# Kernel tuning notes

Measured on AMD Instinct MI355X. Metric: run time of the kernel, lower is better.

## Reference

```python
import jax, jax.numpy as jnp
import numpy as np

B, S, H = 4, 2048, 768          # batch, seq, hidden
NH, HD = 12, 64                 # heads, head dim
R = 4                           # channel_shrink_ratio
LH, LHD = H // R, HD // R       # layout hidden (192), layout head dim (16)


def setup_inputs() -> dict:
    key = jax.random.key(0)
    ks = jax.random.split(key, 14)
    s = 0.02
    return {
        "hidden_states": jax.random.normal(ks[0], (B, S, H), jnp.float32),
        "layout_inputs": jax.random.normal(ks[1], (B, S, LH), jnp.float32),
        # text-stream projections (stored as [in, out], i.e. torch weight transposed)
        "Wq": jax.random.normal(ks[2], (H, H), jnp.float32) * s,
        "bq": jnp.zeros((H,), jnp.float32),
        "Wk": jax.random.normal(ks[3], (H, H), jnp.float32) * s,
        "bk": jnp.zeros((H,), jnp.float32),
        "Wv": jax.random.normal(ks[4], (H, H), jnp.float32) * s,
        "bv": jnp.zeros((H,), jnp.float32),
        # layout-stream projections
        "lWq": jax.random.normal(ks[5], (LH, LH), jnp.float32) * s,
        "lbq": jnp.zeros((LH,), jnp.float32),
        "lWk": jax.random.normal(ks[6], (LH, LH), jnp.float32) * s,
        "lbk": jnp.zeros((LH,), jnp.float32),
        "lWv": jax.random.normal(ks[7], (LH, LH), jnp.float32) * s,
        "lbv": jnp.zeros((LH,), jnp.float32),
    }


def _heads(x, w, b, hd):
    # [B,S,D_in] @ [D_in,D_out] -> [B, NH, S, hd]
    y = x @ w + b
    return y.reshape(x.shape[0], x.shape[1], NH, hd).transpose(0, 2, 1, 3)


def reference(hidden_states, layout_inputs, Wq, bq, Wk, bk, Wv, bv,
              lWq, lbq, lWk, lbk, lWv, lbv):
    q = _heads(hidden_states, Wq, bq, HD)
    k = _heads(hidden_states, Wk, bk, HD)
    v = _heads(hidden_states, Wv, bv, HD)
    lq = _heads(layout_inputs, lWq, lbq, LHD)
    lk = _heads(layout_inputs, lWk, lbk, LHD)
    lv = _heads(layout_inputs, lWv, lbv, LHD)

    # two QK^T score matrices, scaled then cross-added (both streams see the sum)
    scores = jnp.einsum('bhqd,bhkd->bhqk', q, k) / np.float32(HD) ** 0.5
    lscores = jnp.einsum('bhqd,bhkd->bhqk', lq, lk) / np.float32(LHD) ** 0.5
    combined = scores + lscores  # identical for both streams (no mask path)

    probs = jax.nn.softmax(combined, axis=-1)
    lprobs = jax.nn.softmax(combined, axis=-1)

    ctx = jnp.einsum('bhqk,bhkd->bhqd', probs, v)
    lctx = jnp.einsum('bhqk,bhkd->bhqd', lprobs, lv)

    ctx = ctx.transpose(0, 2, 1, 3).reshape(B, S, H)
    lctx = lctx.transpose(0, 2, 1, 3).reshape(B, S, LH)
    return ctx, lctx
```

## Files before the change

kernel.cpp:

```cpp
#include <hip/hip_runtime.h>
#include <cstdint>
#include <cstddef>

#define NB 4
#define NS 2048
#define NHH 12
#define DH 80
#define HT 768
#define HL 192

typedef __bf16 bf16x8 __attribute__((ext_vector_type(8)));
typedef float f32x4 __attribute__((ext_vector_type(4)));
typedef unsigned short u16x4 __attribute__((ext_vector_type(4)));

__device__ __forceinline__ unsigned short f2bf(float f) {
  union { float f; uint32_t u; } v; v.f = f;
  uint32_t u = v.u + 0x7FFF + ((v.u >> 16) & 1);
  return (unsigned short)(u >> 16);
}

__device__ __forceinline__ f32x4 mfma_bf16(bf16x8 a, bf16x8 b, f32x4 c) {
  return __builtin_amdgcn_mfma_f32_16x16x32_bf16(a, b, c, 0, 0, 0);
}

__device__ __forceinline__ void gl_lds(const unsigned short* g, unsigned short* l) {
  __builtin_amdgcn_global_load_lds(
      (const __attribute__((address_space(1))) uint32_t*)g,
      (__attribute__((address_space(3))) uint32_t*)l, 16, 0, 0);
}

__global__ __launch_bounds__(256) void k_prep(
    const float* __restrict__ hs, const float* __restrict__ li,
    const float* __restrict__ Wq, const float* __restrict__ Wk, const float* __restrict__ Wv,
    const float* __restrict__ lWq, const float* __restrict__ lWk, const float* __restrict__ lWv,
    unsigned short* __restrict__ Xb, unsigned short* __restrict__ Xlb,
    unsigned short* __restrict__ WtQ, unsigned short* __restrict__ WtK,
    unsigned short* __restrict__ WtV, unsigned short* __restrict__ WtLQ,
    unsigned short* __restrict__ WtLK, unsigned short* __restrict__ WtLV) {
  int blk = blockIdx.x, tid = threadIdx.x;
  if (blk < 7680) {
    const float* src; unsigned short* dst; int i;
    if (blk < 6144) { src = hs; dst = Xb;  i = blk * 256 + tid; }
    else            { src = li; dst = Xlb; i = (blk - 6144) * 256 + tid; }
    float4 v = *(const float4*)(src + (size_t)i * 4);
    u16x4 o; o[0] = f2bf(v.x); o[1] = f2bf(v.y); o[2] = f2bf(v.z); o[3] = f2bf(v.w);
    *(u16x4*)(dst + (size_t)i * 4) = o;
  } else {
    const float* w; unsigned short* wt; int i, K;
    if      (blk < 9984)  { w = Wq;  wt = WtQ;  i = (blk - 7680)  * 256 + tid; K = 768; }
    else if (blk < 12288) { w = Wk;  wt = WtK;  i = (blk - 9984)  * 256 + tid; K = 768; }
    else if (blk < 14592) { w = Wv;  wt = WtV;  i = (blk - 12288) * 256 + tid; K = 768; }
    else if (blk < 14736) { w = lWq; wt = WtLQ; i = (blk - 14592) * 256 + tid; K = 192; }
    else if (blk < 14880) { w = lWk; wt = WtLK; i = (blk - 14736) * 256 + tid; K = 192; }
    else                  { w = lWv; wt = WtLV; i = (blk - 14880) * 256 + tid; K = 192; }
    int n = i / K, k = i - n * K;
    wt[i] = f2bf(w[(size_t)k * K + n]);
  }
}

struct ProjArgs {
  const unsigned short* Wt[3];
  const float* bias[3];
  unsigned short* dst[3];
  float scale[3];
  int mode[3];
};

__global__ __launch_bounds__(256, 4) void k_proj3(
    const unsigned short* __restrict__ Xb, ProjArgs pa,
    int K, int hdshift, int dofs) {
  __shared__ unsigned short Xs[128 * 72];
  __shared__ unsigned short Ws[64 * 72];
  int z = blockIdx.z;
  const unsigned short* Wt = pa.Wt[z];
  int m0 = blockIdx.x * 128, n0 = blockIdx.y * 64;
  int tid = threadIdx.x;
  int lane = tid & 63, wave = tid >> 6, quad = lane >> 4, l16 = lane & 15;

  f32x4 acc[2][4];
#pragma unroll
  for (int mt = 0; mt < 2; ++mt)
#pragma unroll
    for (int nt = 0; nt < 4; ++nt) {
      acc[mt][nt][0] = 0.f; acc[mt][nt][1] = 0.f;
      acc[mt][nt][2] = 0.f; acc[mt][nt][3] = 0.f;
    }

  for (int kk = 0; kk < K; kk += 64) {
#pragma unroll
    for (int p = 0; p < 5; ++p) {
      int i = p * 256 + tid;
      if (i < 1152) {
        int r = i / 9, c = i - r * 9;
        const unsigned short* src = Xb + (size_t)(m0 + r) * K + kk + (c == 8 ? 0 : c * 8);
        gl_lds(src, Xs + i * 8);
      }
    }
#pragma unroll
    for (int p = 0; p < 3; ++p) {
      int i = p * 256 + tid;
      if (i < 576) {
        int r = i / 9, c = i - r * 9;
        const unsigned short* src = Wt + (size_t)(n0 + r) * K + kk + (c == 8 ? 0 : c * 8);
        gl_lds(src, Ws + i * 8);
      }
    }
    __syncthreads();

#pragma unroll
    for (int kc = 0; kc < 2; ++kc) {
      bf16x8 a0 = *(const bf16x8*)&Xs[(wave * 32 + l16) * 72 + kc * 32 + quad * 8];
      bf16x8 a1 = *(const bf16x8*)&Xs[(wave * 32 + 16 + l16) * 72 + kc * 32 + quad * 8];
#pragma unroll
      for (int nt = 0; nt < 4; ++nt) {
        bf16x8 b = *(const bf16x8*)&Ws[(nt * 16 + l16) * 72 + kc * 32 + quad * 8];
        acc[0][nt] = mfma_bf16(a0, b, acc[0][nt]);
        acc[1][nt] = mfma_bf16(a1, b, acc[1][nt]);
      }
    }
    __syncthreads();
  }

  const float* bias = pa.bias[z];
  unsigned short* dst = pa.dst[z];
  float scale = pa.scale[z];
  int mode = pa.mode[z];
  int hdm = (1 << hdshift) - 1;
#pragma unroll
  for (int mt = 0; mt < 2; ++mt) {
#pragma unroll
    for (int nt = 0; nt < 4; ++nt) {
      int n = n0 + nt * 16 + l16;
      float bv = bias[n];
      int mbase = m0 + wave * 32 + mt * 16 + quad * 4;
      int h = n >> hdshift, d = n & hdm;
      if (mode == 0) {
#pragma unroll
        for (int r = 0; r < 4; ++r) {
          int m = mbase + r;
          int b = m >> 11, s = m & (NS - 1);
          float y = (acc[mt][nt][r] + bv) * scale;
          dst[((size_t)(b * NHH + h) * NS + s) * DH + dofs + d] = f2bf(y);
        }
      } else {
        int b = mbase >> 11, s = mbase & (NS - 1);
        u16x4 pk;
#pragma unroll
        for (int r = 0; r < 4; ++r) pk[r] = f2bf((acc[mt][nt][r] + bv) * scale);
        *(u16x4*)(dst + ((size_t)(b * NHH + h) * DH + dofs + d) * NS + s) = pk;
      }
    }
  }
}

__global__ __launch_bounds__(256, 3) void k_attn(
    const unsigned short* __restrict__ Qg, const unsigned short* __restrict__ Kg,
    const unsigned short* __restrict__ Vg,
    float* __restrict__ outT, float* __restrict__ outL) {
  __shared__ unsigned short Kt[64 * 80];
  __shared__ unsigned short Vt[80 * 72];
  __shared__ unsigned short Pt[128 * 72];
  __shared__ float rowsum[128];

  int tid = threadIdx.x;
  int lane = tid & 63, wave = tid >> 6, quad = lane >> 4, l16 = lane & 15;
  int bb = blockIdx.z, hh = blockIdx.y, bh = bb * NHH + hh;
  int q0 = blockIdx.x * 128;

  bf16x8 qf[2][3];
#pragma unroll
  for (int mt = 0; mt < 2; ++mt) {
    const unsigned short* qrow =
        Qg + ((size_t)bh * NS + q0 + wave * 32 + mt * 16 + l16) * DH;
#pragma unroll
    for (int kc = 0; kc < 3; ++kc) {
      if (kc == 2 && quad >= 2) {
#pragma unroll
        for (int j = 0; j < 8; ++j) qf[mt][kc][j] = (__bf16)0.0f;
      } else {
        qf[mt][kc] = *(const bf16x8*)(qrow + kc * 32 + quad * 8);
      }
    }
  }

  f32x4 o[2][5];
#pragma unroll
  for (int om = 0; om < 2; ++om)
#pragma unroll
    for (int nt = 0; nt < 5; ++nt) {
      o[om][nt][0] = 0.f; o[om][nt][1] = 0.f; o[om][nt][2] = 0.f; o[om][nt][3] = 0.f;
    }
  float rs[2] = {0.f, 0.f};

  const unsigned short* kbase0 = Kg + (size_t)bh * NS * DH;
  const unsigned short* vrow = Vg + (size_t)bh * DH * NS;

  for (int kt = 0; kt < NS / 64; ++kt) {
    int k0 = kt * 64;
    const unsigned short* kbase = kbase0 + (size_t)k0 * DH;
    gl_lds(kbase + (size_t)tid * 8, Kt + tid * 8);
    gl_lds(kbase + (size_t)(256 + tid) * 8, Kt + (256 + tid) * 8);
    if (tid < 128) gl_lds(kbase + (size_t)(512 + tid) * 8, Kt + (512 + tid) * 8);
#pragma unroll
    for (int p = 0; p < 3; ++p) {
      int i = p * 256 + tid;
      if (i < 720) {
        int r = i / 9, c = i - r * 9;
        const unsigned short* src = (c == 8) ? vrow : (vrow + (size_t)r * NS + k0 + c * 8);
        gl_lds(src, Vt + i * 8);
      }
    }
    __syncthreads();

    f32x4 st[2][4];
#pragma unroll
    for (int mt = 0; mt < 2; ++mt)
#pragma unroll
      for (int nt = 0; nt < 4; ++nt) {
        st[mt][nt][0] = 0.f; st[mt][nt][1] = 0.f; st[mt][nt][2] = 0.f; st[mt][nt][3] = 0.f;
      }
#pragma unroll
    for (int kc = 0; kc < 3; ++kc) {
#pragma unroll
      for (int nt = 0; nt < 4; ++nt) {
        bf16x8 a = *(const bf16x8*)&Kt[(nt * 16 + l16) * 80 + kc * 32 + quad * 8];
        st[0][nt] = mfma_bf16(a, qf[0][kc], st[0][nt]);
        st[1][nt] = mfma_bf16(a, qf[1][kc], st[1][nt]);
      }
    }

#pragma unroll
    for (int mt = 0; mt < 2; ++mt) {
      unsigned short* prow = &Pt[(wave * 32 + mt * 16 + l16) * 72];
#pragma unroll
      for (int nt = 0; nt < 4; ++nt) {
        float e0 = __expf(st[mt][nt][0]);
        float e1 = __expf(st[mt][nt][1]);
        float e2 = __expf(st[mt][nt][2]);
        float e3 = __expf(st[mt][nt][3]);
        rs[mt] += (e0 + e1) + (e2 + e3);
        u16x4 pk; pk[0] = f2bf(e0); pk[1] = f2bf(e1); pk[2] = f2bf(e2); pk[3] = f2bf(e3);
        *(u16x4*)(prow + nt * 16 + quad * 4) = pk;
      }
    }

#pragma unroll
    for (int kc = 0; kc < 2; ++kc) {
      bf16x8 a0 = *(const bf16x8*)&Pt[(wave * 32 + l16) * 72 + kc * 32 + quad * 8];
      bf16x8 a1 = *(const bf16x8*)&Pt[(wave * 32 + 16 + l16) * 72 + kc * 32 + quad * 8];
#pragma unroll
      for (int nt = 0; nt < 5; ++nt) {
        bf16x8 b = *(const bf16x8*)&Vt[(nt * 16 + l16) * 72 + kc * 32 + quad * 8];
        o[0][nt] = mfma_bf16(a0, b, o[0][nt]);
        o[1][nt] = mfma_bf16(a1, b, o[1][nt]);
      }
    }
    __syncthreads();
  }

#pragma unroll
  for (int mt = 0; mt < 2; ++mt) {
    rs[mt] += __shfl_xor(rs[mt], 16);
    rs[mt] += __shfl_xor(rs[mt], 32);
    if (quad == 0) rowsum[wave * 32 + mt * 16 + l16] = rs[mt];
  }
  __syncthreads();

#pragma unroll
  for (int om = 0; om < 2; ++om) {
#pragma unroll
    for (int r = 0; r < 4; ++r) {
      int row = wave * 32 + om * 16 + quad * 4 + r;
      float inv = 1.0f / rowsum[row];
      int s = q0 + row;
#pragma unroll
      for (int nt = 0; nt < 4; ++nt)
        outT[((size_t)bb * NS + s) * HT + hh * 64 + nt * 16 + l16] = o[om][nt][r] * inv;
      outL[((size_t)bb * NS + s) * HL + hh * 16 + l16] = o[om][4][r] * inv;
    }
  }
}

extern "C" void kernel_launch(void* const* d_in, const int* in_sizes, int n_in,
                              void* d_out, int out_size, void* d_ws, size_t ws_size,
                              hipStream_t stream) {
  const float* hs  = (const float*)d_in[0];
  const float* li  = (const float*)d_in[1];
  const float* Wq  = (const float*)d_in[2];
  const float* bq  = (const float*)d_in[3];
  const float* Wk  = (const float*)d_in[4];
  const float* bk  = (const float*)d_in[5];
  const float* Wv  = (const float*)d_in[6];
  const float* bv  = (const float*)d_in[7];
  const float* lWq = (const float*)d_in[8];
  const float* lbq = (const float*)d_in[9];
  const float* lWk = (const float*)d_in[10];
  const float* lbk = (const float*)d_in[11];
  const float* lWv = (const float*)d_in[12];
  const float* lbv = (const float*)d_in[13];

  char* ws = (char*)d_ws;
  size_t off = 0;
  auto alloc = [&](size_t bytes) {
    char* p = ws + off;
    off += (bytes + 255) & ~(size_t)255;
    return (unsigned short*)p;
  };
  unsigned short* Xb   = alloc((size_t)8192 * 768 * 2);
  unsigned short* Xlb  = alloc((size_t)8192 * 192 * 2);
  unsigned short* WtQ  = alloc((size_t)768 * 768 * 2);
  unsigned short* WtK  = alloc((size_t)768 * 768 * 2);
  unsigned short* WtV  = alloc((size_t)768 * 768 * 2);
  unsigned short* WtLQ = alloc((size_t)192 * 192 * 2);
  unsigned short* WtLK = alloc((size_t)192 * 192 * 2);
  unsigned short* WtLV = alloc((size_t)192 * 192 * 2);
  unsigned short* Qs   = alloc((size_t)NB * NHH * NS * DH * 2);
  unsigned short* Ks   = alloc((size_t)NB * NHH * NS * DH * 2);
  unsigned short* Vs   = alloc((size_t)NB * NHH * NS * DH * 2 + 256);

  k_prep<<<15024, 256, 0, stream>>>(hs, li, Wq, Wk, Wv, lWq, lWk, lWv,
                                    Xb, Xlb, WtQ, WtK, WtV, WtLQ, WtLK, WtLV);

  const float s8 = 0.35355339059327373f;
  const float s4 = 0.5f;
  {
    ProjArgs pa;
    pa.Wt[0] = WtQ; pa.Wt[1] = WtK; pa.Wt[2] = WtV;
    pa.bias[0] = bq; pa.bias[1] = bk; pa.bias[2] = bv;
    pa.dst[0] = Qs; pa.dst[1] = Ks; pa.dst[2] = Vs;
    pa.scale[0] = s8; pa.scale[1] = s8; pa.scale[2] = 1.f;
    pa.mode[0] = 0; pa.mode[1] = 0; pa.mode[2] = 1;
    k_proj3<<<dim3(64, 12, 3), 256, 0, stream>>>(Xb, pa, 768, 6, 0);
  }
  {
    ProjArgs pa;
    pa.Wt[0] = WtLQ; pa.Wt[1] = WtLK; pa.Wt[2] = WtLV;
    pa.bias[0] = lbq; pa.bias[1] = lbk; pa.bias[2] = lbv;
    pa.dst[0] = Qs; pa.dst[1] = Ks; pa.dst[2] = Vs;
    pa.scale[0] = s4; pa.scale[1] = s4; pa.scale[2] = 1.f;
    pa.mode[0] = 0; pa.mode[1] = 0; pa.mode[2] = 1;
    k_proj3<<<dim3(64, 3, 3), 256, 0, stream>>>(Xlb, pa, 192, 4, 64);
  }
  float* outT = (float*)d_out;
  float* outL = outT + (size_t)NB * NS * HT;
  k_attn<<<dim3(16, 12, 4), 256, 0, stream>>>(Qs, Ks, Vs, outT, outL);
}
```

Measured before the change: 260.9 us.

## Restructure attention to keep P in registers, double-buffer K/V, fold rowsum into MFMA

The attention kernel now double-buffers K and V tiles in LDS so the next tile's loads overlap compute. It keeps exp'd probabilities in registers as fp16 and computes the P·V product as V^T·P^T with f16 MFMA, which removes the P round-trip through LDS. The row sum is obtained by an extra V row of ones, so the separate reduction and the rowsum LDS array go away, and outputs are written as float4. Separately, weight transposes use an LDS-tiled coalesced transpose, the text projection uses wider 128-column tiles, and conversions use hardware casts. V is stored in fp16 instead of bf16, trading some range for mantissa precision.

After: 255.1 us. -2.2%, faster.

```diff
diff --git a/kernel.cpp b/kernel.cpp
--- a/kernel.cpp
+++ b/kernel.cpp
@@ -10,17 +10,29 @@
 #define HL 192
 
 typedef __bf16 bf16x8 __attribute__((ext_vector_type(8)));
+typedef _Float16 f16x4 __attribute__((ext_vector_type(4)));
+typedef _Float16 f16x2 __attribute__((ext_vector_type(2)));
 typedef float f32x4 __attribute__((ext_vector_type(4)));
 typedef unsigned short u16x4 __attribute__((ext_vector_type(4)));
 
-__device__ __forceinline__ unsigned short f2bf(float f) {
-  union { float f; uint32_t u; } v; v.f = f;
-  uint32_t u = v.u + 0x7FFF + ((v.u >> 16) & 1);
-  return (unsigned short)(u >> 16);
-}
-
-__device__ __forceinline__ f32x4 mfma_bf16(bf16x8 a, bf16x8 b, f32x4 c) {
+__device__ __forceinline__ unsigned short bfc(float f) {
+  __bf16 b = (__bf16)f;
+  return __builtin_bit_cast(unsigned short, b);
+}
+__device__ __forceinline__ unsigned short f16c(float f) {
+  _Float16 h = (_Float16)f;
+  return __builtin_bit_cast(unsigned short, h);
+}
+
+__device__ __forceinline__ f32x4 mfma_bf16_k32(bf16x8 a, bf16x8 b, f32x4 c) {
   return __builtin_amdgcn_mfma_f32_16x16x32_bf16(a, b, c, 0, 0, 0);
+}
+__device__ __forceinline__ f32x4 mfma_f16_k16(f16x4 a, f16x4 b, f32x4 c) {
+  return __builtin_amdgcn_mfma_f32_16x16x16f16(a, b, c, 0, 0, 0);
+}
+
+__device__ __forceinline__ f16x2 pk_f16(float a, float b) {
+  return __builtin_bit_cast(f16x2, __builtin_amdgcn_cvt_pkrtz(a, b));
 }
 
 __device__ __forceinline__ void gl_lds(const unsigned short* g, unsigned short* l) {
@@ -37,24 +49,36 @@
     unsigned short* __restrict__ WtQ, unsigned short* __restrict__ WtK,
     unsigned short* __restrict__ WtV, unsigned short* __restrict__ WtLQ,
     unsigned short* __restrict__ WtLK, unsigned short* __restrict__ WtLV) {
+  __shared__ float Ts[32][33];
   int blk = blockIdx.x, tid = threadIdx.x;
   if (blk < 7680) {
     const float* src; unsigned short* dst; int i;
     if (blk < 6144) { src = hs; dst = Xb;  i = blk * 256 + tid; }
     else            { src = li; dst = Xlb; i = (blk - 6144) * 256 + tid; }
     float4 v = *(const float4*)(src + (size_t)i * 4);
-    u16x4 o; o[0] = f2bf(v.x); o[1] = f2bf(v.y); o[2] = f2bf(v.z); o[3] = f2bf(v.w);
+    u16x4 o; o[0] = bfc(v.x); o[1] = bfc(v.y); o[2] = bfc(v.z); o[3] = bfc(v.w);
     *(u16x4*)(dst + (size_t)i * 4) = o;
   } else {
-    const float* w; unsigned short* wt; int i, K;
-    if      (blk < 9984)  { w = Wq;  wt = WtQ;  i = (blk - 7680)  * 256 + tid; K = 768; }
-    else if (blk < 12288) { w = Wk;  wt = WtK;  i = (blk - 9984)  * 256 + tid; K = 768; }
-    else if (blk < 14592) { w = Wv;  wt = WtV;  i = (blk - 12288) * 256 + tid; K = 768; }
-    else if (blk < 14736) { w = lWq; wt = WtLQ; i = (blk - 14592) * 256 + tid; K = 192; }
-    else if (blk < 14880) { w = lWk; wt = WtLK; i = (blk - 14736) * 256 + tid; K = 192; }
-    else                  { w = lWv; wt = WtLV; i = (blk - 14880) * 256 + tid; K = 192; }
-    int n = i / K, k = i - n * K;
-    wt[i] = f2bf(w[(size_t)k * K + n]);
+    const float* w; unsigned short* wt; int t, K;
+    if (blk < 9408) {
+      int b2 = blk - 7680; int m = b2 / 576; t = b2 - m * 576; K = 768;
+      w  = (m == 0) ? Wq  : (m == 1) ? Wk  : Wv;
+      wt = (m == 0) ? WtQ : (m == 1) ? WtK : WtV;
+    } else {
+      int b2 = blk - 9408; int m = b2 / 36; t = b2 - m * 36; K = 192;
+      w  = (m == 0) ? lWq  : (m == 1) ? lWk  : lWv;
+      wt = (m == 0) ? WtLQ : (m == 1) ? WtLK : WtLV;
+    }
+    int TB = K >> 5;
+    int kb = t / TB, nb = t - kb * TB;
+    int tx = tid & 31, ty = tid >> 5;
+#pragma unroll
+    for (int j = 0; j < 4; ++j)
+      Ts[ty + j * 8][tx] = w[(size_t)(kb * 32 + ty + j * 8) * K + nb * 32 + tx];
+    __syncthreads();
+#pragma unroll
+    for (int j = 0; j < 4; ++j)
+      wt[(size_t)(nb * 32 + ty + j * 8) * K + kb * 32 + tx] = bfc(Ts[tx][ty + j * 8]);
   }
 }
 
@@ -66,43 +90,45 @@
   int mode[3];
 };
 
-__global__ __launch_bounds__(256, 4) void k_proj3(
+template<int NT>
+__global__ __launch_bounds__(256, 4) void k_proj(
     const unsigned short* __restrict__ Xb, ProjArgs pa,
     int K, int hdshift, int dofs) {
+  constexpr int BN = NT * 16;
   __shared__ unsigned short Xs[128 * 72];
-  __shared__ unsigned short Ws[64 * 72];
+  __shared__ unsigned short Ws[BN * 72];
   int z = blockIdx.z;
   const unsigned short* Wt = pa.Wt[z];
-  int m0 = blockIdx.x * 128, n0 = blockIdx.y * 64;
+  int m0 = blockIdx.x * 128, n0 = blockIdx.y * BN;
   int tid = threadIdx.x;
   int lane = tid & 63, wave = tid >> 6, quad = lane >> 4, l16 = lane & 15;
 
-  f32x4 acc[2][4];
+  f32x4 acc[2][NT];
 #pragma unroll
   for (int mt = 0; mt < 2; ++mt)
 #pragma unroll
-    for (int nt = 0; nt < 4; ++nt) {
+    for (int nt = 0; nt < NT; ++nt) {
       acc[mt][nt][0] = 0.f; acc[mt][nt][1] = 0.f;
       acc[mt][nt][2] = 0.f; acc[mt][nt][3] = 0.f;
     }
 
   for (int kk = 0; kk < K; kk += 64) {
-#pragma unroll
-    for (int p = 0; p < 5; ++p) {
+    constexpr int XCH = 128 * 9;
+#pragma unroll
+    for (int p = 0; p < (XCH + 255) / 256; ++p) {
       int i = p * 256 + tid;
-      if (i < 1152) {
+      if (i < XCH) {
         int r = i / 9, c = i - r * 9;
-        const unsigned short* src = Xb + (size_t)(m0 + r) * K + kk + (c == 8 ? 0 : c * 8);
-        gl_lds(src, Xs + i * 8);
-      }
-    }
-#pragma unroll
-    for (int p = 0; p < 3; ++p) {
+        gl_lds(Xb + (size_t)(m0 + r) * K + kk + (c == 8 ? 0 : c * 8), Xs + i * 8);
+      }
+    }
+    constexpr int WCH = BN * 9;
+#pragma unroll
+    for (int p = 0; p < (WCH + 255) / 256; ++p) {
       int i = p * 256 + tid;
-      if (i < 576) {
+      if (i < WCH) {
         int r = i / 9, c = i - r * 9;
-        const unsigned short* src = Wt + (size_t)(n0 + r) * K + kk + (c == 8 ? 0 : c * 8);
-        gl_lds(src, Ws + i * 8);
+        gl_lds(Wt + (size_t)(n0 + r) * K + kk + (c == 8 ? 0 : c * 8), Ws + i * 8);
       }
     }
     __syncthreads();
@@ -112,10 +138,10 @@
       bf16x8 a0 = *(const bf16x8*)&Xs[(wave * 32 + l16) * 72 + kc * 32 + quad * 8];
       bf16x8 a1 = *(const bf16x8*)&Xs[(wave * 32 + 16 + l16) * 72 + kc * 32 + quad * 8];
 #pragma unroll
-      for (int nt = 0; nt < 4; ++nt) {
+      for (int nt = 0; nt < NT; ++nt) {
         bf16x8 b = *(const bf16x8*)&Ws[(nt * 16 + l16) * 72 + kc * 32 + quad * 8];
-        acc[0][nt] = mfma_bf16(a0, b, acc[0][nt]);
-        acc[1][nt] = mfma_bf16(a1, b, acc[1][nt]);
+        acc[0][nt] = mfma_bf16_k32(a0, b, acc[0][nt]);
+        acc[1][nt] = mfma_bf16_k32(a1, b, acc[1][nt]);
       }
     }
     __syncthreads();
@@ -129,7 +155,7 @@
 #pragma unroll
   for (int mt = 0; mt < 2; ++mt) {
 #pragma unroll
-    for (int nt = 0; nt < 4; ++nt) {
+    for (int nt = 0; nt < NT; ++nt) {
       int n = n0 + nt * 16 + l16;
       float bv = bias[n];
       int mbase = m0 + wave * 32 + mt * 16 + quad * 4;
@@ -139,14 +165,14 @@
         for (int r = 0; r < 4; ++r) {
           int m = mbase + r;
           int b = m >> 11, s = m & (NS - 1);
-          float y = (acc[mt][nt][r] + bv) * scale;
-          dst[((size_t)(b * NHH + h) * NS + s) * DH + dofs + d] = f2bf(y);
+          dst[((size_t)(b * NHH + h) * NS + s) * DH + dofs + d] =
+              bfc((acc[mt][nt][r] + bv) * scale);
         }
       } else {
         int b = mbase >> 11, s = mbase & (NS - 1);
         u16x4 pk;
 #pragma unroll
-        for (int r = 0; r < 4; ++r) pk[r] = f2bf((acc[mt][nt][r] + bv) * scale);
+        for (int r = 0; r < 4; ++r) pk[r] = f16c((acc[mt][nt][r] + bv) * scale);
         *(u16x4*)(dst + ((size_t)(b * NHH + h) * DH + dofs + d) * NS + s) = pk;
       }
     }
@@ -157,16 +183,22 @@
     const unsigned short* __restrict__ Qg, const unsigned short* __restrict__ Kg,
     const unsigned short* __restrict__ Vg,
     float* __restrict__ outT, float* __restrict__ outL) {
-  __shared__ unsigned short Kt[64 * 80];
-  __shared__ unsigned short Vt[80 * 72];
-  __shared__ unsigned short Pt[128 * 72];
-  __shared__ float rowsum[128];
+  __shared__ unsigned short KT[2][64 * 88];
+  __shared__ unsigned short VT[2][96 * 72];
 
   int tid = threadIdx.x;
   int lane = tid & 63, wave = tid >> 6, quad = lane >> 4, l16 = lane & 15;
   int bb = blockIdx.z, hh = blockIdx.y, bh = bb * NHH + hh;
   int q0 = blockIdx.x * 128;
 
+  const unsigned short* kg0 = Kg + (size_t)bh * NS * DH;
+  const unsigned short* vg0 = Vg + (size_t)bh * DH * NS;
+
+  for (int i = tid; i < 2304; i += 256) {
+    int b = i / 1152, j = i - b * 1152;
+    VT[b][80 * 72 + j] = (j < 72) ? (unsigned short)0x3C00 : (unsigned short)0;
+  }
+
   bf16x8 qf[2][3];
 #pragma unroll
   for (int mt = 0; mt < 2; ++mt) {
@@ -183,34 +215,46 @@
     }
   }
 
-  f32x4 o[2][5];
-#pragma unroll
-  for (int om = 0; om < 2; ++om)
-#pragma unroll
-    for (int nt = 0; nt < 5; ++nt) {
-      o[om][nt][0] = 0.f; o[om][nt][1] = 0.f; o[om][nt][2] = 0.f; o[om][nt][3] = 0.f;
-    }
-  float rs[2] = {0.f, 0.f};
-
-  const unsigned short* kbase0 = Kg + (size_t)bh * NS * DH;
-  const unsigned short* vrow = Vg + (size_t)bh * DH * NS;
-
-  for (int kt = 0; kt < NS / 64; ++kt) {
+  f32x4 o[2][6];
+#pragma unroll
+  for (int mt = 0; mt < 2; ++mt)
+#pragma unroll
+    for (int vt = 0; vt < 6; ++vt) {
+      o[mt][vt][0] = 0.f; o[mt][vt][1] = 0.f; o[mt][vt][2] = 0.f; o[mt][vt][3] = 0.f;
+    }
+
+  auto stage = [&](int buf, int kt) {
+    const unsigned short* kb = kg0 + (size_t)kt * 64 * DH;
+    unsigned short* dk = &KT[buf][0];
+#pragma unroll
+    for (int p = 0; p < 3; ++p) {
+      int i = p * 256 + tid;
+      if (i < 704) {
+        int r = i / 11, c = i - r * 11;
+        gl_lds(kb + (size_t)r * DH + (c == 10 ? 0 : c * 8), dk + i * 8);
+      }
+    }
     int k0 = kt * 64;
-    const unsigned short* kbase = kbase0 + (size_t)k0 * DH;
-    gl_lds(kbase + (size_t)tid * 8, Kt + tid * 8);
-    gl_lds(kbase + (size_t)(256 + tid) * 8, Kt + (256 + tid) * 8);
-    if (tid < 128) gl_lds(kbase + (size_t)(512 + tid) * 8, Kt + (512 + tid) * 8);
+    unsigned short* dv = &VT[buf][0];
 #pragma unroll
     for (int p = 0; p < 3; ++p) {
       int i = p * 256 + tid;
       if (i < 720) {
         int r = i / 9, c = i - r * 9;
-        const unsigned short* src = (c == 8) ? vrow : (vrow + (size_t)r * NS + k0 + c * 8);
-        gl_lds(src, Vt + i * 8);
-      }
-    }
+        gl_lds((c == 8) ? vg0 : (vg0 + (size_t)r * NS + k0 + c * 8), dv + i * 8);
+      }
+    }
+  };
+
+  stage(0, 0);
+
+  for (int kt = 0; kt < 32; ++kt) {
+    int cur = kt & 1;
     __syncthreads();
+    if (kt + 1 < 32) stage(cur ^ 1, kt + 1);
+
+    const unsigned short* Kc = &KT[cur][0];
+    const unsigned short* Vc = &VT[cur][0];
 
     f32x4 st[2][4];
 #pragma unroll
@@ -223,61 +267,52 @@
     for (int kc = 0; kc < 3; ++kc) {
 #pragma unroll
       for (int nt = 0; nt < 4; ++nt) {
-        bf16x8 a = *(const bf16x8*)&Kt[(nt * 16 + l16) * 80 + kc * 32 + quad * 8];
-        st[0][nt] = mfma_bf16(a, qf[0][kc], st[0][nt]);
-        st[1][nt] = mfma_bf16(a, qf[1][kc], st[1][nt]);
-      }
-    }
-
-#pragma unroll
-    for (int mt = 0; mt < 2; ++mt) {
-      unsigned short* prow = &Pt[(wave * 32 + mt * 16 + l16) * 72];
+        bf16x8 a = *(const bf16x8*)&Kc[(nt * 16 + l16) * 88 + kc * 32 + quad * 8];
+        st[0][nt] = mfma_bf16_k32(a, qf[0][kc], st[0][nt]);
+        st[1][nt] = mfma_bf16_k32(a, qf[1][kc], st[1][nt]);
+      }
+    }
+
+    f16x4 pf[2][4];
+#pragma unroll
+    for (int mt = 0; mt < 2; ++mt)
 #pragma unroll
       for (int nt = 0; nt < 4; ++nt) {
-        float e0 = __expf(st[mt][nt][0]);
-        float e1 = __expf(st[mt][nt][1]);
-        float e2 = __expf(st[mt][nt][2]);
-        float e3 = __expf(st[mt][nt][3]);
-        rs[mt] += (e0 + e1) + (e2 + e3);
-        u16x4 pk; pk[0] = f2bf(e0); pk[1] = f2bf(e1); pk[2] = f2bf(e2); pk[3] = f2bf(e3);
-        *(u16x4*)(prow + nt * 16 + quad * 4) = pk;
-      }
-    }
-
-#pragma unroll
-    for (int kc = 0; kc < 2; ++kc) {
-      bf16x8 a0 = *(const bf16x8*)&Pt[(wave * 32 + l16) * 72 + kc * 32 + quad * 8];
-      bf16x8 a1 = *(const bf16x8*)&Pt[(wave * 32 + 16 + l16) * 72 + kc * 32 + quad * 8];
-#pragma unroll
-      for (int nt = 0; nt < 5; ++nt) {
-        bf16x8 b = *(const bf16x8*)&Vt[(nt * 16 + l16) * 72 + kc * 32 + quad * 8];
-        o[0][nt] = mfma_bf16(a0, b, o[0][nt]);
-        o[1][nt] = mfma_bf16(a1, b, o[1][nt]);
-      }
-    }
-    __syncthreads();
+        f16x2 lo = pk_f16(__expf(st[mt][nt][0]), __expf(st[mt][nt][1]));
+        f16x2 hi = pk_f16(__expf(st[mt][nt][2]), __expf(st[mt][nt][3]));
+        union { f16x4 v; f16x2 h[2]; } u;
+        u.h[0] = lo; u.h[1] = hi;
+        pf[mt][nt] = u.v;
+      }
+
+#pragma unroll
+    for (int nt = 0; nt < 4; ++nt) {
+#pragma unroll
+      for (int vt = 0; vt < 6; ++vt) {
+        f16x4 va = *(const f16x4*)&Vc[(vt * 16 + l16) * 72 + nt * 16 + quad * 4];
+        o[0][vt] = mfma_f16_k16(va, pf[0][nt], o[0][vt]);
+        o[1][vt] = mfma_f16_k16(va, pf[1][nt], o[1][vt]);
+      }
+    }
   }
 
 #pragma unroll
   for (int mt = 0; mt < 2; ++mt) {
-    rs[mt] += __shfl_xor(rs[mt], 16);
-    rs[mt] += __shfl_xor(rs[mt], 32);
-    if (quad == 0) rowsum[wave * 32 + mt * 16 + l16] = rs[mt];
-  }
-  __syncthreads();
-
-#pragma unroll
-  for (int om = 0; om < 2; ++om) {
-#pragma unroll
-    for (int r = 0; r < 4; ++r) {
-      int row = wave * 32 + om * 16 + quad * 4 + r;
-      float inv = 1.0f / rowsum[row];
-      int s = q0 + row;
-#pragma unroll
-      for (int nt = 0; nt < 4; ++nt)
-        outT[((size_t)bb * NS + s) * HT + hh * 64 + nt * 16 + l16] = o[om][nt][r] * inv;
-      outL[((size_t)bb * NS + s) * HL + hh * 16 + l16] = o[om][4][r] * inv;
-    }
+    float rsum = __shfl(o[mt][5][0], l16);
+    float inv = 1.0f / rsum;
+    int s = q0 + wave * 32 + mt * 16 + l16;
+    float* baseT = outT + ((size_t)bb * NS + s) * HT + hh * 64 + quad * 4;
+#pragma unroll
+    for (int vt = 0; vt < 4; ++vt) {
+      float4 v4;
+      v4.x = o[mt][vt][0] * inv; v4.y = o[mt][vt][1] * inv;
+      v4.z = o[mt][vt][2] * inv; v4.w = o[mt][vt][3] * inv;
+      *(float4*)(baseT + vt * 16) = v4;
+    }
+    float4 vl;
+    vl.x = o[mt][4][0] * inv; vl.y = o[mt][4][1] * inv;
+    vl.z = o[mt][4][2] * inv; vl.w = o[mt][4][3] * inv;
+    *(float4*)(outL + ((size_t)bb * NS + s) * HL + hh * 16 + quad * 4) = vl;
   }
 }
 
@@ -318,8 +353,8 @@
   unsigned short* Ks   = alloc((size_t)NB * NHH * NS * DH * 2);
   unsigned short* Vs   = alloc((size_t)NB * NHH * NS * DH * 2 + 256);
 
-  k_prep<<<15024, 256, 0, stream>>>(hs, li, Wq, Wk, Wv, lWq, lWk, lWv,
-                                    Xb, Xlb, WtQ, WtK, WtV, WtLQ, WtLK, WtLV);
+  k_prep<<<9516, 256, 0, stream>>>(hs, li, Wq, Wk, Wv, lWq, lWk, lWv,
+                                   Xb, Xlb, WtQ, WtK, WtV, WtLQ, WtLK, WtLV);
 
   const float s8 = 0.35355339059327373f;
   const float s4 = 0.5f;
@@ -330,7 +365,7 @@
     pa.dst[0] = Qs; pa.dst[1] = Ks; pa.dst[2] = Vs;
     pa.scale[0] = s8; pa.scale[1] = s8; pa.scale[2] = 1.f;
     pa.mode[0] = 0; pa.mode[1] = 0; pa.mode[2] = 1;
-    k_proj3<<<dim3(64, 12, 3), 256, 0, stream>>>(Xb, pa, 768, 6, 0);
+    k_proj<8><<<dim3(64, 6, 3), 256, 0, stream>>>(Xb, pa, 768, 6, 0);
   }
   {
     ProjArgs pa;
@@ -339,7 +374,7 @@
     pa.dst[0] = Qs; pa.dst[1] = Ks; pa.dst[2] = Vs;
     pa.scale[0] = s4; pa.scale[1] = s4; pa.scale[2] = 1.f;
     pa.mode[0] = 0; pa.mode[1] = 0; pa.mode[2] = 1;
-    k_proj3<<<dim3(64, 3, 3), 256, 0, stream>>>(Xlb, pa, 192, 4, 64);
+    k_proj<4><<<dim3(64, 3, 3), 256, 0, stream>>>(Xlb, pa, 192, 4, 64);
   }
   float* outT = (float*)d_out;
   float* outL = outT + (size_t)NB * NS * HT;
```
